# Performance work log

Measured on AMD Instinct MI355X. Metric: run time of the kernel, lower is better.

The kernel has to match this reference:

```python
import jax, jax.numpy as jnp
import numpy as np

DIM = 128
NUM_HEADS = 2
HEAD_DIM = DIM // NUM_HEADS
SCALE = HEAD_DIM ** -0.5
SR = 4
EPS_LN = 1e-5


def token2map(x, idx_token, H, W, H_init, W_init):
    """Scatter tokens x[B,N,Cc] into a [B,Cc,H,W] map via the init grid.
    Matches the sparse-COO branch of the torch token2map (N_init < N*H*W).
    """
    B, N, Cc = x.shape
    N_init = H_init * W_init
    # nearest-neighbor index of each init-grid cell in the HxW map
    rows = (jnp.arange(H_init) * H) // H_init          # floor(i * H / H_init)
    cols = (jnp.arange(W_init) * W) // W_init
    idx_hw = (rows[:, None] * W + cols[None, :]).reshape(-1)      # [N_init]
    flat = (idx_hw[None, :] + jnp.arange(B)[:, None] * (H * W)).reshape(-1)  # [B*N_init]
    # per-pixel count (A @ ones) + 1e-6, as in torch
    count = jax.ops.segment_sum(jnp.ones((B * N_init,), jnp.float32), flat,
                                num_segments=B * H * W) + 1e-6    # [B*H*W]
    gathered = jnp.take_along_axis(x, idx_token[..., None], axis=1)  # [B,N_init,Cc]
    out = jax.ops.segment_sum(gathered.reshape(B * N_init, Cc), flat,
                              num_segments=B * H * W)
    out = out / count[:, None]
    return out.reshape(B, H, W, Cc).transpose(0, 3, 1, 2)  # [B,Cc,H,W]


def setup_inputs() -> dict:
    key = jax.random.key(0)
    ks = jax.random.split(key, 12)
    B, Nq, Nkv, C = 8, 12544, 12544, DIM
    H, W, H_init, W_init = 112, 112, 224, 224
    inp = {
        'q_x': jax.random.normal(ks[0], (B, Nq, C), jnp.float32),
        'kv_x': jax.random.normal(ks[1], (B, Nkv, C), jnp.float32),
        'token_score': jax.random.normal(ks[2], (B, Nkv, 1), jnp.float32),
        'idx_token': jax.random.randint(ks[3], (B, H_init * W_init), 0, Nkv),
        'H': H, 'W': W, 'H_init': H_init, 'W_init': W_init,
        # learned params (qkv_bias=False)
        'q_w': jax.random.normal(ks[4], (C, C), jnp.float32) * 0.02,
        'kv_w': jax.random.normal(ks[5], (C, 2 * C), jnp.float32) * 0.02,
        'proj_w': jax.random.normal(ks[6], (C, C), jnp.float32) * 0.02,
        'proj_b': jnp.zeros((C,), jnp.float32),
        'sr_w': jax.random.normal(ks[7], (C, C, SR, SR), jnp.float32) * np.sqrt(2.0 / (SR * SR * C)),
        'sr_b': jnp.zeros((C,), jnp.float32),
        'norm_g': jnp.ones((C,), jnp.float32),
        'norm_b': jnp.zeros((C,), jnp.float32),
    }
    return inp


def reference(q_x, kv_x, token_score, q_w, kv_w, proj_w, proj_b, sr_w, sr_b,
              norm_g, norm_b, idx_token, H, W, H_init, W_init):
    B, Nq, C = q_x.shape
    # q projection -> [B, h, Nq, d]
    q = (q_x @ q_w).reshape(B, Nq, NUM_HEADS, HEAD_DIM).transpose(0, 2, 1, 3)

    # sr_ratio > 1 path: scatter kv tokens (with conf channel) to q's map
    tmp = jnp.concatenate([kv_x, token_score], axis=-1)          # [B,Nkv,C+1]
    tmp_map = token2map(tmp, idx_token, H, W, H_init, W_init)    # [B,C+1,H,W]
    kv_map = tmp_map[:, :C]                                      # [B,C,H,W]
    conf_map = tmp_map[:, C:]                                    # [B,1,H,W]

    # spatial reduction conv (kernel=stride=SR) + LayerNorm
    kv_r = jax.lax.conv_general_dilated(
        kv_map, sr_w, window_strides=(SR, SR), padding='VALID',
        dimension_numbers=('NCHW', 'OIHW', 'NCHW')) + sr_b[None, :, None, None]
    h, w = kv_r.shape[2], kv_r.shape[3]
    Ns = h * w
    kv_t = kv_r.reshape(B, C, Ns).transpose(0, 2, 1)             # [B,Ns,C]
    mu = jnp.mean(kv_t, axis=-1, keepdims=True)
    var = jnp.mean(jnp.square(kv_t - mu), axis=-1, keepdims=True)
    kv_t = (kv_t - mu) / jnp.sqrt(var + EPS_LN) * norm_g + norm_b

    # avg-pool conf to the reduced grid
    conf = conf_map.reshape(B, 1, h, SR, w, SR).mean(axis=(3, 5)).reshape(B, Ns)

    # kv projection -> k,v [B,h,Ns,d]
    kv_p = (kv_t @ kv_w).reshape(B, Ns, 2, NUM_HEADS, HEAD_DIM).transpose(2, 0, 3, 1, 4)
    k, v = kv_p[0], kv_p[1]

    attn = jnp.einsum('bhqd,bhkd->bhqk', q * SCALE, k) + conf[:, None, None, :]
    attn = jax.nn.softmax(attn, axis=-1)
    out = jnp.einsum('bhqk,bhkd->bhqd', attn, v).transpose(0, 2, 1, 3).reshape(B, Nq, C)
    return out @ proj_w + proj_b
```

## Files before the change

### kernel.cpp

```cpp
#include <hip/hip_runtime.h>
#include <hip/hip_bf16.h>


#define NBATCH 8
#define NQTOK  12544
#define NSP    832
#define LOG2E  1.4426950408889634f
#define QSCALE (0.125f * LOG2E)

typedef __attribute__((ext_vector_type(8))) short bf8;
typedef __attribute__((ext_vector_type(4))) float f4;
typedef __attribute__((ext_vector_type(4))) unsigned short u16x4;
typedef __attribute__((ext_vector_type(2))) unsigned int u32x2;

#define MFMA16(a, b, c) __builtin_amdgcn_mfma_f32_16x16x32_bf16((a), (b), (c), 0, 0, 0)

#if __has_builtin(__builtin_amdgcn_exp2f)
#define EXP2(x) __builtin_amdgcn_exp2f(x)
#else
#define EXP2(x) exp2f(x)
#endif

__device__ __forceinline__ unsigned short f2b(float x) {
  union { float f; unsigned u; } v; v.f = x;
  unsigned r = v.u + 0x7FFFu + ((v.u >> 16) & 1u);
  return (unsigned short)(r >> 16);
}

__device__ __forceinline__ unsigned pk2(float lo, float hi) {
  float2 t; t.x = lo; t.y = hi;
  __hip_bfloat162 bb = __float22bfloat162_rn(t);
  union { __hip_bfloat162 b; unsigned u; } v; v.b = bb;
  return v.u;
}

__device__ __forceinline__ bf8 ldfrag(const unsigned short* t, int stride, int rbase, int kbase) {
  int lane = threadIdx.x & 63;
  return *(const bf8*)(t + (rbase + (lane & 15)) * stride + kbase + ((lane >> 4) << 3));
}

__global__ void k_setup(const float* __restrict__ qw, const float* __restrict__ kvw,
                        const float* __restrict__ pw, const float* __restrict__ srw,
                        unsigned short* __restrict__ qwt, unsigned short* __restrict__ kvwt,
                        unsigned short* __restrict__ pwt, unsigned short* __restrict__ srwt,
                        unsigned* __restrict__ kb, unsigned* __restrict__ vb,
                        float* __restrict__ conf) {
  int tid = blockIdx.x * 256 + threadIdx.x;
  int nt = gridDim.x * 256;
  for (int i = tid; i < 128 * 128; i += nt) {
    int k = i >> 7, n = i & 127;
    qwt[n * 128 + k] = f2b(qw[k * 128 + n]);
    pwt[n * 128 + k] = f2b(pw[k * 128 + n]);
  }
  for (int i = tid; i < 128 * 256; i += nt) {
    int k = i >> 8, j = i & 255;
    kvwt[j * 128 + k] = f2b(kvw[k * 256 + j]);
  }
  for (int i = tid; i < 128 * 2048; i += nt) {
    int o = i >> 11, kk = i & 2047;
    int p = kk >> 7, c = kk & 127;
    srwt[o * 2048 + kk] = f2b(srw[o * 2048 + c * 16 + p]);
  }
  const int nu = NBATCH * 2 * NSP * 64 / 2;
  for (int i = tid; i < nu; i += nt) { kb[i] = 0u; vb[i] = 0u; }
  for (int i = tid; i < NBATCH * NSP; i += nt) conf[i] = -1e30f;
}

__global__ void k_token2map(const float* __restrict__ kv_x, const float* __restrict__ tsc,
                            const int* __restrict__ idxt,
                            unsigned short* __restrict__ kv_map, float* __restrict__ conf_map) {
  int half = threadIdx.x >> 7;
  int c = threadIdx.x & 127;
  int cell = blockIdx.x * 2 + half;
  int b = cell / 12544, hw = cell - b * 12544;
  int h = hw / 112, w = hw - h * 112;
  const int* it = idxt + b * 50176;
  int t0 = it[(2 * h) * 224 + 2 * w];
  int t1 = it[(2 * h) * 224 + 2 * w + 1];
  int t2 = it[(2 * h + 1) * 224 + 2 * w];
  int t3 = it[(2 * h + 1) * 224 + 2 * w + 1];
  const float* base = kv_x + (long)b * 12544 * 128;
  const float recip = 1.0f / (4.0f + 1e-6f);
  float s = base[t0 * 128 + c] + base[t1 * 128 + c] + base[t2 * 128 + c] + base[t3 * 128 + c];
  kv_map[(long)cell * 128 + c] = f2b(s * recip);
  if (c == 0) {
    const float* ts = tsc + b * 12544;
    conf_map[cell] = (ts[t0] + ts[t1] + ts[t2] + ts[t3]) * recip;
  }
}

__launch_bounds__(256)
__global__ void k_conv_ln(const unsigned short* __restrict__ kv_map,
                          const unsigned short* __restrict__ srwt,
                          const float* __restrict__ srb, const float* __restrict__ ng,
                          const float* __restrict__ nb, unsigned short* __restrict__ kv_t,
                          const float* __restrict__ conf_map, float* __restrict__ conf) {
  __shared__ unsigned short At[64 * 136];
  __shared__ unsigned short Bt[128 * 136];
  const int tid = threadIdx.x;
  const int lane = tid & 63, w = tid >> 6;
  const int l15 = lane & 15, g = lane >> 4;
  const int r0 = blockIdx.x * 64;
  if (tid < 64) {
    int pos = r0 + tid;
    int bq = pos / 784, p2 = pos - bq * 784;
    int oh = p2 / 28, ow = p2 - oh * 28;
    float s = 0.f;
#pragma unroll
    for (int kh = 0; kh < 4; kh++)
#pragma unroll
      for (int kw = 0; kw < 4; kw++)
        s += conf_map[bq * 12544 + (4 * oh + kh) * 112 + 4 * ow + kw];
    conf[bq * NSP + p2] = s * (LOG2E / 16.0f);
  }
  const f4 fz = {0.f, 0.f, 0.f, 0.f};
  f4 acc[8];
#pragma unroll
  for (int i = 0; i < 8; i++) acc[i] = fz;

  for (int p = 0; p < 16; p++) {
#pragma unroll
    for (int j = 0; j < 4; j++) {
      int id = tid + 256 * j;
      int row = id >> 4, c0 = (id & 15) << 3;
      int rr = r0 + row;
      int bb = rr / 784, pos = rr - bb * 784;
      int oh = pos / 28, ow = pos - oh * 28;
      long src = ((long)(bb * 12544 + (4 * oh + (p >> 2)) * 112 + 4 * ow + (p & 3))) * 128 + c0;
      *(uint4*)(At + row * 136 + c0) = *(const uint4*)(kv_map + src);
    }
#pragma unroll
    for (int j = 0; j < 8; j++) {
      int id = tid + 256 * j;
      int row = id >> 4, c0 = (id & 15) << 3;
      *(uint4*)(Bt + row * 136 + c0) = *(const uint4*)(srwt + row * 2048 + p * 128 + c0);
    }
    __syncthreads();
#pragma unroll
    for (int ks = 0; ks < 4; ks++) {
      bf8 a = ldfrag(At, 136, 16 * w, 32 * ks);
#pragma unroll
      for (int nf = 0; nf < 8; nf++) {
        bf8 bb = ldfrag(Bt, 136, 16 * nf, 32 * ks);
        acc[nf] = MFMA16(a, bb, acc[nf]);
      }
    }
    __syncthreads();
  }
  float sum_[4] = {0.f, 0.f, 0.f, 0.f}, sq_[4] = {0.f, 0.f, 0.f, 0.f};
#pragma unroll
  for (int nf = 0; nf < 8; nf++) {
    float bias = srb[16 * nf + l15];
#pragma unroll
    for (int reg = 0; reg < 4; reg++) {
      float v = acc[nf][reg] + bias;
      acc[nf][reg] = v;
      sum_[reg] += v;
      sq_[reg] += v * v;
    }
  }
#pragma unroll
  for (int msk = 1; msk < 16; msk <<= 1)
#pragma unroll
    for (int reg = 0; reg < 4; reg++) {
      sum_[reg] += __shfl_xor(sum_[reg], msk, 64);
      sq_[reg] += __shfl_xor(sq_[reg], msk, 64);
    }
  float mean[4], rstd[4];
#pragma unroll
  for (int reg = 0; reg < 4; reg++) {
    mean[reg] = sum_[reg] * (1.0f / 128.0f);
    float var = sq_[reg] * (1.0f / 128.0f) - mean[reg] * mean[reg];
    rstd[reg] = rsqrtf(var + 1e-5f);
  }
#pragma unroll
  for (int nf = 0; nf < 8; nf++) {
    float gc = ng[16 * nf + l15], bc = nb[16 * nf + l15];
#pragma unroll
    for (int reg = 0; reg < 4; reg++) {
      int row = r0 + 16 * w + 4 * g + reg;
      float v = (acc[nf][reg] - mean[reg]) * rstd[reg] * gc + bc;
      kv_t[row * 128 + 16 * nf + l15] = f2b(v);
    }
  }
}

__launch_bounds__(256)
__global__ void k_kv(const unsigned short* __restrict__ kv_t,
                     const unsigned short* __restrict__ kvwt,
                     unsigned short* __restrict__ kbuf, unsigned short* __restrict__ vbuf) {
  __shared__ unsigned short At[64 * 136];
  __shared__ unsigned short Bt[128 * 136];
  const int tid = threadIdx.x;
  const int lane = tid & 63, w = tid >> 6;
  const int l15 = lane & 15, g = lane >> 4;
  const int r0 = blockIdx.x * 64;
  const int sel = blockIdx.y;
#pragma unroll
  for (int j = 0; j < 4; j++) {
    int id = tid + 256 * j;
    int row = id >> 4, c0 = (id & 15) << 3;
    *(uint4*)(At + row * 136 + c0) = *(const uint4*)(kv_t + (long)(r0 + row) * 128 + c0);
  }
#pragma unroll
  for (int j = 0; j < 8; j++) {
    int id = tid + 256 * j;
    int row = id >> 4, c0 = (id & 15) << 3;
    *(uint4*)(Bt + row * 136 + c0) = *(const uint4*)(kvwt + (long)(sel * 128 + row) * 128 + c0);
  }
  __syncthreads();
  const f4 fz = {0.f, 0.f, 0.f, 0.f};
  f4 acc[8];
#pragma unroll
  for (int i = 0; i < 8; i++) acc[i] = fz;
#pragma unroll
  for (int ks = 0; ks < 4; ks++) {
    bf8 a = ldfrag(At, 136, 16 * w, 32 * ks);
#pragma unroll
    for (int nf = 0; nf < 8; nf++) {
      bf8 bb = ldfrag(Bt, 136, 16 * nf, 32 * ks);
      acc[nf] = MFMA16(a, bb, acc[nf]);
    }
  }
#pragma unroll
  for (int nf = 0; nf < 8; nf++)
#pragma unroll
    for (int reg = 0; reg < 4; reg++) {
      int r = r0 + 16 * w + 4 * g + reg;
      int b = r / 784, ns = r - b * 784;
      int j = 16 * nf + l15;
      int hh = j >> 6, d = j & 63;
      unsigned short val = f2b(acc[nf][reg]);
      if (sel == 0) kbuf[((long)(b * 2 + hh) * NSP + ns) * 64 + d] = val;
      else          vbuf[((long)(b * 2 + hh) * 64 + d) * NSP + ns] = val;
    }
}

__launch_bounds__(256)
__global__ void k_q(const float* __restrict__ q_x, const unsigned short* __restrict__ qwt,
                    unsigned short* __restrict__ qbuf) {
  __shared__ unsigned short At[64 * 136];
  __shared__ unsigned short Bt[128 * 136];
  const int tid = threadIdx.x;
  const int lane = tid & 63, w = tid >> 6;
  const int l15 = lane & 15, g = lane >> 4;
  const int r0 = blockIdx.x * 64;
#pragma unroll
  for (int j = 0; j < 8; j++) {
    int id = tid + 256 * j;
    int row = id >> 5, c0 = (id & 31) << 2;
    float4 v = *(const float4*)(q_x + (long)(r0 + row) * 128 + c0);
    u16x4 o;
    o[0] = f2b(v.x); o[1] = f2b(v.y); o[2] = f2b(v.z); o[3] = f2b(v.w);
    *(u16x4*)(At + row * 136 + c0) = o;
  }
#pragma unroll
  for (int j = 0; j < 8; j++) {
    int id = tid + 256 * j;
    int row = id >> 4, c0 = (id & 15) << 3;
    *(uint4*)(Bt + row * 136 + c0) = *(const uint4*)(qwt + (long)row * 128 + c0);
  }
  __syncthreads();
  const f4 fz = {0.f, 0.f, 0.f, 0.f};
  f4 acc[8];
#pragma unroll
  for (int i = 0; i < 8; i++) acc[i] = fz;
#pragma unroll
  for (int ks = 0; ks < 4; ks++) {
    bf8 a = ldfrag(At, 136, 16 * w, 32 * ks);
#pragma unroll
    for (int nf = 0; nf < 8; nf++) {
      bf8 bb = ldfrag(Bt, 136, 16 * nf, 32 * ks);
      acc[nf] = MFMA16(a, bb, acc[nf]);
    }
  }
#pragma unroll
  for (int nf = 0; nf < 8; nf++)
#pragma unroll
    for (int reg = 0; reg < 4; reg++) {
      int r = r0 + 16 * w + 4 * g + reg;
      int b = r / NQTOK, n = r - b * NQTOK;
      int j = 16 * nf + l15;
      int hh = j >> 6, d = j & 63;
      qbuf[((long)(b * 2 + hh) * NQTOK + n) * 64 + d] = f2b(acc[nf][reg] * QSCALE);
    }
}

__launch_bounds__(256, 3)
__global__ void k_attn(const unsigned short* __restrict__ qbuf,
                       const unsigned short* __restrict__ kbuf,
                       const unsigned short* __restrict__ vbuf,
                       const float* __restrict__ conf,
                       unsigned short* __restrict__ attbuf) {
  __shared__ unsigned short Kt[2][64 * 72];
  __shared__ unsigned short Vt[2][64 * 72];
  const int tid = threadIdx.x;
  const int lane = tid & 63, w = tid >> 6;
  const int l15 = lane & 15, g = lane >> 4;
  const int h = blockIdx.y, b = blockIdx.z;
  const int bh = b * 2 + h;
  const int q0 = blockIdx.x * 128 + 32 * w;

  const unsigned short* qsrc = qbuf + ((long)bh * NQTOK + q0) * 64;
  bf8 qf[2][2];
#pragma unroll
  for (int mr = 0; mr < 2; mr++)
#pragma unroll
    for (int ks = 0; ks < 2; ks++)
      qf[mr][ks] = *(const bf8*)(qsrc + (16 * mr + l15) * 64 + 32 * ks + (g << 3));

  const int srow = tid >> 2;
  const int scol = (tid & 3) << 4;
  const unsigned short* kg = kbuf + (long)bh * NSP * 64 + srow * 64 + scol;
  const unsigned short* vg = vbuf + (long)bh * 64 * NSP + (long)srow * NSP + scol;
  unsigned short* klds = &Kt[0][0] + srow * 72 + scol;
  unsigned short* vlds = &Vt[0][0] + srow * 72 + scol;

  uint4 kr0, kr1, vr0, vr1;
#define ISSUE(T)                                                   \
  do {                                                             \
    const unsigned short* kp_ = kg + (long)(T) * 4096;             \
    const unsigned short* vp_ = vg + (T) * 64;                     \
    kr0 = *(const uint4*)(kp_);                                    \
    kr1 = *(const uint4*)(kp_ + 8);                                \
    vr0 = *(const uint4*)(vp_);                                    \
    vr1 = *(const uint4*)(vp_ + 8);                                \
  } while (0)
#define STWRITE(BUF)                                               \
  do {                                                             \
    unsigned short* kd_ = klds + (BUF) * 4608;                     \
    unsigned short* vd_ = vlds + (BUF) * 4608;                     \
    *(uint4*)kd_ = kr0;  *(uint4*)(kd_ + 8) = kr1;                 \
    *(uint4*)vd_ = vr0;  *(uint4*)(vd_ + 8) = vr1;                 \
  } while (0)

  ISSUE(0);
  STWRITE(0);
  ISSUE(1);
  __syncthreads();

  const f4 fz = {0.f, 0.f, 0.f, 0.f};
  f4 ao[2][4], aol[2];
#pragma unroll
  for (int mr = 0; mr < 2; mr++) {
    aol[mr] = fz;
#pragma unroll
    for (int i = 0; i < 4; i++) ao[mr][i] = fz;
  }
  const short on = (short)0x3F80;
  const bf8 onesf = {on, on, on, on, on, on, on, on};
  const float* confb = conf + b * NSP;

#pragma unroll 2
  for (int t = 0; t < 13; t++) {
    const int cur = t & 1;
    const unsigned short* KtB = &Kt[cur][0];
    const unsigned short* VtB = &Vt[cur][0];
    bf8 kf[4][2];
#pragma unroll
    for (int mf = 0; mf < 4; mf++)
#pragma unroll
      for (int ks = 0; ks < 2; ks++)
        kf[mf][ks] = ldfrag(KtB, 72, 16 * mf, 32 * ks);
    bf8 vf[4][2];
#pragma unroll
    for (int nfd = 0; nfd < 4; nfd++)
#pragma unroll
      for (int ks = 0; ks < 2; ks++)
        vf[nfd][ks] = ldfrag(VtB, 72, 16 * nfd, 32 * ks);
    float4 cv[4];
#pragma unroll
    for (int mf = 0; mf < 4; mf++)
      cv[mf] = *(const float4*)(confb + t * 64 + 16 * mf + 4 * g);
#pragma unroll
    for (int mr = 0; mr < 2; mr++) {
      f4 s_[4];
#pragma unroll
      for (int mf = 0; mf < 4; mf++) s_[mf] = fz;
#pragma unroll
      for (int ks = 0; ks < 2; ks++)
#pragma unroll
        for (int mf = 0; mf < 4; mf++)
          s_[mf] = MFMA16(kf[mf][ks], qf[mr][ks], s_[mf]);
      unsigned W[4][2];
#pragma unroll
      for (int mf = 0; mf < 4; mf++) {
        float p0 = EXP2(s_[mf][0] + cv[mf].x);
        float p1 = EXP2(s_[mf][1] + cv[mf].y);
        float p2 = EXP2(s_[mf][2] + cv[mf].z);
        float p3 = EXP2(s_[mf][3] + cv[mf].w);
        W[mf][0] = pk2(p0, p1);
        W[mf][1] = pk2(p2, p3);
      }
#pragma unroll
      for (int ks = 0; ks < 2; ks++) {
        u32x2 r0 = __builtin_amdgcn_permlane32_swap(W[2 * ks][0], W[2 * ks + 1][0], false, false);
        u32x2 t02 = __builtin_amdgcn_permlane16_swap(r0.x, r0.y, false, false);
        u32x2 r1 = __builtin_amdgcn_permlane32_swap(W[2 * ks][1], W[2 * ks + 1][1], false, false);
        u32x2 t13 = __builtin_amdgcn_permlane16_swap(r1.x, r1.y, false, false);
        union { unsigned u[4]; bf8 v; } pa;
        pa.u[0] = t02.x; pa.u[1] = t13.x; pa.u[2] = t02.y; pa.u[3] = t13.y;
        aol[mr] = MFMA16(pa.v, onesf, aol[mr]);
#pragma unroll
        for (int nfd = 0; nfd < 4; nfd++)
          ao[mr][nfd] = MFMA16(pa.v, vf[nfd][ks], ao[mr][nfd]);
      }
    }
    if (t < 12) STWRITE(cur ^ 1);
    if (t < 11) ISSUE(t + 2);
    __syncthreads();
  }
#undef ISSUE
#undef STWRITE
#pragma unroll
  for (int mr = 0; mr < 2; mr++) {
    float inv[4];
#pragma unroll
    for (int reg = 0; reg < 4; reg++) inv[reg] = 1.0f / aol[mr][reg];
#pragma unroll
    for (int nfd = 0; nfd < 4; nfd++)
#pragma unroll
      for (int reg = 0; reg < 4; reg++) {
        int n = q0 + 16 * mr + 4 * g + reg;
        int col = h * 64 + 16 * nfd + l15;
        attbuf[((long)b * NQTOK + n) * 128 + col] = f2b(ao[mr][nfd][reg] * inv[reg]);
      }
  }
}

__launch_bounds__(256)
__global__ void k_proj(const unsigned short* __restrict__ attbuf,
                       const unsigned short* __restrict__ pwt,
                       const float* __restrict__ pb, float* __restrict__ out) {
  __shared__ unsigned short At[64 * 136];
  __shared__ unsigned short Bt[128 * 136];
  const int tid = threadIdx.x;
  const int lane = tid & 63, w = tid >> 6;
  const int l15 = lane & 15, g = lane >> 4;
  const int r0 = blockIdx.x * 64;
#pragma unroll
  for (int j = 0; j < 4; j++) {
    int id = tid + 256 * j;
    int row = id >> 4, c0 = (id & 15) << 3;
    *(uint4*)(At + row * 136 + c0) = *(const uint4*)(attbuf + (long)(r0 + row) * 128 + c0);
  }
#pragma unroll
  for (int j = 0; j < 8; j++) {
    int id = tid + 256 * j;
    int row = id >> 4, c0 = (id & 15) << 3;
    *(uint4*)(Bt + row * 136 + c0) = *(const uint4*)(pwt + (long)row * 128 + c0);
  }
  __syncthreads();
  const f4 fz = {0.f, 0.f, 0.f, 0.f};
  f4 acc[8];
#pragma unroll
  for (int i = 0; i < 8; i++) acc[i] = fz;
#pragma unroll
  for (int ks = 0; ks < 4; ks++) {
    bf8 a = ldfrag(At, 136, 16 * w, 32 * ks);
#pragma unroll
    for (int nf = 0; nf < 8; nf++) {
      bf8 bb = ldfrag(Bt, 136, 16 * nf, 32 * ks);
      acc[nf] = MFMA16(a, bb, acc[nf]);
    }
  }
#pragma unroll
  for (int nf = 0; nf < 8; nf++) {
    float bias = pb[16 * nf + l15];
#pragma unroll
    for (int reg = 0; reg < 4; reg++) {
      int r = r0 + 16 * w + 4 * g + reg;
      out[(long)r * 128 + 16 * nf + l15] = acc[nf][reg] + bias;
    }
  }
}

extern "C" void kernel_launch(void* const* d_in, const int* in_sizes, int n_in,
                              void* d_out, int out_size, void* d_ws, size_t ws_size,
                              hipStream_t stream) {
  const float* q_x  = (const float*)d_in[0];
  const float* kv_x = (const float*)d_in[1];
  const float* tsc  = (const float*)d_in[2];
  const int*   idxt = (const int*)d_in[3];
  const float* q_w  = (const float*)d_in[8];
  const float* kv_w = (const float*)d_in[9];
  const float* pw   = (const float*)d_in[10];
  const float* pb   = (const float*)d_in[11];
  const float* srw  = (const float*)d_in[12];
  const float* srb  = (const float*)d_in[13];
  const float* ng   = (const float*)d_in[14];
  const float* nb   = (const float*)d_in[15];
  float* outp = (float*)d_out;

  char* ws = (char*)d_ws;
  size_t off = 0;
  auto take = [&](size_t bytes) {
    char* p = ws + off;
    off += (bytes + 255) & ~(size_t)255;
    return p;
  };
  unsigned short* qwt   = (unsigned short*)take(128 * 128 * 2);
  unsigned short* pwt   = (unsigned short*)take(128 * 128 * 2);
  unsigned short* kvwt  = (unsigned short*)take(256 * 128 * 2);
  unsigned short* srwt  = (unsigned short*)take(128 * 2048 * 2);
  unsigned short* kvmap = (unsigned short*)take((size_t)NBATCH * 12544 * 128 * 2);
  float* conf_map       = (float*)take((size_t)NBATCH * 12544 * 4);
  unsigned short* kvt   = (unsigned short*)take((size_t)NBATCH * 784 * 128 * 2);
  unsigned short* kbuf  = (unsigned short*)take((size_t)NBATCH * 2 * NSP * 64 * 2);
  unsigned short* vbuf  = (unsigned short*)take((size_t)NBATCH * 2 * NSP * 64 * 2);
  float* conf           = (float*)take((size_t)NBATCH * NSP * 4);
  unsigned short* qbuf  = (unsigned short*)take((size_t)NBATCH * 2 * NQTOK * 64 * 2);
  unsigned short* attbuf = kvmap;

  k_setup<<<512, 256, 0, stream>>>(q_w, kv_w, pw, srw, qwt, kvwt, pwt, srwt,
                                   (unsigned*)kbuf, (unsigned*)vbuf, conf);
  k_token2map<<<50176, 256, 0, stream>>>(kv_x, tsc, idxt, kvmap, conf_map);
  k_conv_ln<<<98, 256, 0, stream>>>(kvmap, srwt, srb, ng, nb, kvt, conf_map, conf);
  k_kv<<<dim3(98, 2), 256, 0, stream>>>(kvt, kvwt, kbuf, vbuf);
  k_q<<<1568, 256, 0, stream>>>(q_x, qwt, qbuf);
  k_attn<<<dim3(98, 2, 8), 256, 0, stream>>>(qbuf, kbuf, vbuf, conf, attbuf);
  k_proj<<<1568, 256, 0, stream>>>(attbuf, pwt, pb, outp);
}
```

Before: 178.4 us.

## Fuse conv+LN with KV projection, vectorize token2map, remap attention blocks to XCDs

Merges the conv+LayerNorm kernel with the KV projection, so normalized rows stay in shared memory and B fragments come straight from global memory, dropping one launch and the kv_t round trip. token2map now uses float4 loads with 32 threads per cell and batch-interleaved block ids, and the Q scale is folded into the transposed weight. Attention blocks use a 1-D grid mapped so that each XCD handles one batch's two heads, aiming to improve L2 locality of K/V. The fused kernel keeps more accumulators (16 f4), which raises register pressure.

```diff
diff --git a/kernel.cpp b/kernel.cpp
--- a/kernel.cpp
+++ b/kernel.cpp
@@ -32,6 +32,16 @@
   __hip_bfloat162 bb = __float22bfloat162_rn(t);
   union { __hip_bfloat162 b; unsigned u; } v; v.b = bb;
   return v.u;
+}
+
+__device__ __forceinline__ bf8 rows2frag(const unsigned W0[2], const unsigned W1[2]) {
+  u32x2 r0 = __builtin_amdgcn_permlane32_swap(W0[0], W1[0], false, false);
+  u32x2 t02 = __builtin_amdgcn_permlane16_swap(r0.x, r0.y, false, false);
+  u32x2 r1 = __builtin_amdgcn_permlane32_swap(W0[1], W1[1], false, false);
+  u32x2 t13 = __builtin_amdgcn_permlane16_swap(r1.x, r1.y, false, false);
+  union { unsigned u[4]; bf8 v; } pa;
+  pa.u[0] = t02.x; pa.u[1] = t13.x; pa.u[2] = t02.y; pa.u[3] = t13.y;
+  return pa.v;
 }
 
 __device__ __forceinline__ bf8 ldfrag(const unsigned short* t, int stride, int rbase, int kbase) {
@@ -49,7 +59,7 @@
   int nt = gridDim.x * 256;
   for (int i = tid; i < 128 * 128; i += nt) {
     int k = i >> 7, n = i & 127;
-    qwt[n * 128 + k] = f2b(qw[k * 128 + n]);
+    qwt[n * 128 + k] = f2b(qw[k * 128 + n] * QSCALE);
     pwt[n * 128 + k] = f2b(pw[k * 128 + n]);
   }
   for (int i = tid; i < 128 * 256; i += nt) {
@@ -69,32 +79,45 @@
 __global__ void k_token2map(const float* __restrict__ kv_x, const float* __restrict__ tsc,
                             const int* __restrict__ idxt,
                             unsigned short* __restrict__ kv_map, float* __restrict__ conf_map) {
-  int half = threadIdx.x >> 7;
-  int c = threadIdx.x & 127;
-  int cell = blockIdx.x * 2 + half;
-  int b = cell / 12544, hw = cell - b * 12544;
+  int tid = threadIdx.x;
+  int bid = blockIdx.x;
+  int b = bid & 7, pos = bid >> 3;
+  int hw = pos * 8 + (tid >> 5);
+  int cell = b * 12544 + hw;
+  int c0 = (tid & 31) << 2;
   int h = hw / 112, w = hw - h * 112;
   const int* it = idxt + b * 50176;
   int t0 = it[(2 * h) * 224 + 2 * w];
   int t1 = it[(2 * h) * 224 + 2 * w + 1];
   int t2 = it[(2 * h + 1) * 224 + 2 * w];
   int t3 = it[(2 * h + 1) * 224 + 2 * w + 1];
-  const float* base = kv_x + (long)b * 12544 * 128;
+  const float* base = kv_x + (long)b * 12544 * 128 + c0;
   const float recip = 1.0f / (4.0f + 1e-6f);
-  float s = base[t0 * 128 + c] + base[t1 * 128 + c] + base[t2 * 128 + c] + base[t3 * 128 + c];
-  kv_map[(long)cell * 128 + c] = f2b(s * recip);
-  if (c == 0) {
+  float4 a0 = *(const float4*)(base + (long)t0 * 128);
+  float4 a1 = *(const float4*)(base + (long)t1 * 128);
+  float4 a2 = *(const float4*)(base + (long)t2 * 128);
+  float4 a3 = *(const float4*)(base + (long)t3 * 128);
+  u16x4 o;
+  o[0] = f2b((a0.x + a1.x + a2.x + a3.x) * recip);
+  o[1] = f2b((a0.y + a1.y + a2.y + a3.y) * recip);
+  o[2] = f2b((a0.z + a1.z + a2.z + a3.z) * recip);
+  o[3] = f2b((a0.w + a1.w + a2.w + a3.w) * recip);
+  *(u16x4*)(kv_map + (long)cell * 128 + c0) = o;
+  if ((tid & 31) == 0) {
     const float* ts = tsc + b * 12544;
     conf_map[cell] = (ts[t0] + ts[t1] + ts[t2] + ts[t3]) * recip;
   }
 }
 
 __launch_bounds__(256)
-__global__ void k_conv_ln(const unsigned short* __restrict__ kv_map,
-                          const unsigned short* __restrict__ srwt,
-                          const float* __restrict__ srb, const float* __restrict__ ng,
-                          const float* __restrict__ nb, unsigned short* __restrict__ kv_t,
-                          const float* __restrict__ conf_map, float* __restrict__ conf) {
+__global__ void k_conv_ln_kv(const unsigned short* __restrict__ kv_map,
+                             const unsigned short* __restrict__ srwt,
+                             const float* __restrict__ srb, const float* __restrict__ ng,
+                             const float* __restrict__ nb,
+                             const unsigned short* __restrict__ kvwt,
+                             unsigned short* __restrict__ kbuf,
+                             unsigned short* __restrict__ vbuf,
+                             const float* __restrict__ conf_map, float* __restrict__ conf) {
   __shared__ unsigned short At[64 * 136];
   __shared__ unsigned short Bt[128 * 136];
   const int tid = threadIdx.x;
@@ -166,71 +189,39 @@
       sum_[reg] += __shfl_xor(sum_[reg], msk, 64);
       sq_[reg] += __shfl_xor(sq_[reg], msk, 64);
     }
-  float mean[4], rstd[4];
-#pragma unroll
-  for (int reg = 0; reg < 4; reg++) {
-    mean[reg] = sum_[reg] * (1.0f / 128.0f);
-    float var = sq_[reg] * (1.0f / 128.0f) - mean[reg] * mean[reg];
-    rstd[reg] = rsqrtf(var + 1e-5f);
-  }
 #pragma unroll
   for (int nf = 0; nf < 8; nf++) {
     float gc = ng[16 * nf + l15], bc = nb[16 * nf + l15];
 #pragma unroll
     for (int reg = 0; reg < 4; reg++) {
-      int row = r0 + 16 * w + 4 * g + reg;
-      float v = (acc[nf][reg] - mean[reg]) * rstd[reg] * gc + bc;
-      kv_t[row * 128 + 16 * nf + l15] = f2b(v);
-    }
-  }
-}
-
-__launch_bounds__(256)
-__global__ void k_kv(const unsigned short* __restrict__ kv_t,
-                     const unsigned short* __restrict__ kvwt,
-                     unsigned short* __restrict__ kbuf, unsigned short* __restrict__ vbuf) {
-  __shared__ unsigned short At[64 * 136];
-  __shared__ unsigned short Bt[128 * 136];
-  const int tid = threadIdx.x;
-  const int lane = tid & 63, w = tid >> 6;
-  const int l15 = lane & 15, g = lane >> 4;
-  const int r0 = blockIdx.x * 64;
-  const int sel = blockIdx.y;
-#pragma unroll
-  for (int j = 0; j < 4; j++) {
-    int id = tid + 256 * j;
-    int row = id >> 4, c0 = (id & 15) << 3;
-    *(uint4*)(At + row * 136 + c0) = *(const uint4*)(kv_t + (long)(r0 + row) * 128 + c0);
-  }
-#pragma unroll
-  for (int j = 0; j < 8; j++) {
-    int id = tid + 256 * j;
-    int row = id >> 4, c0 = (id & 15) << 3;
-    *(uint4*)(Bt + row * 136 + c0) = *(const uint4*)(kvwt + (long)(sel * 128 + row) * 128 + c0);
+      float mean = sum_[reg] * (1.0f / 128.0f);
+      float var = sq_[reg] * (1.0f / 128.0f) - mean * mean;
+      float v = (acc[nf][reg] - mean) * rsqrtf(var + 1e-5f) * gc + bc;
+      At[(16 * w + 4 * g + reg) * 136 + 16 * nf + l15] = f2b(v);
+    }
   }
   __syncthreads();
-  const f4 fz = {0.f, 0.f, 0.f, 0.f};
-  f4 acc[8];
-#pragma unroll
-  for (int i = 0; i < 8; i++) acc[i] = fz;
+  f4 acc2[16];
+#pragma unroll
+  for (int i = 0; i < 16; i++) acc2[i] = fz;
 #pragma unroll
   for (int ks = 0; ks < 4; ks++) {
     bf8 a = ldfrag(At, 136, 16 * w, 32 * ks);
 #pragma unroll
-    for (int nf = 0; nf < 8; nf++) {
-      bf8 bb = ldfrag(Bt, 136, 16 * nf, 32 * ks);
-      acc[nf] = MFMA16(a, bb, acc[nf]);
-    }
-  }
-#pragma unroll
-  for (int nf = 0; nf < 8; nf++)
+    for (int nf = 0; nf < 16; nf++) {
+      bf8 bb = *(const bf8*)(kvwt + (16 * nf + l15) * 128 + 32 * ks + (g << 3));
+      acc2[nf] = MFMA16(a, bb, acc2[nf]);
+    }
+  }
+#pragma unroll
+  for (int nf = 0; nf < 16; nf++)
 #pragma unroll
     for (int reg = 0; reg < 4; reg++) {
       int r = r0 + 16 * w + 4 * g + reg;
       int b = r / 784, ns = r - b * 784;
       int j = 16 * nf + l15;
-      int hh = j >> 6, d = j & 63;
-      unsigned short val = f2b(acc[nf][reg]);
+      int sel = j >> 7, hh = (j >> 6) & 1, d = j & 63;
+      unsigned short val = f2b(acc2[nf][reg]);
       if (sel == 0) kbuf[((long)(b * 2 + hh) * NSP + ns) * 64 + d] = val;
       else          vbuf[((long)(b * 2 + hh) * 64 + d) * NSP + ns] = val;
     }
@@ -282,7 +273,7 @@
       int b = r / NQTOK, n = r - b * NQTOK;
       int j = 16 * nf + l15;
       int hh = j >> 6, d = j & 63;
-      qbuf[((long)(b * 2 + hh) * NQTOK + n) * 64 + d] = f2b(acc[nf][reg] * QSCALE);
+      qbuf[((long)(b * 2 + hh) * NQTOK + n) * 64 + d] = f2b(acc[nf][reg]);
     }
 }
 
@@ -297,9 +288,14 @@
   const int tid = threadIdx.x;
   const int lane = tid & 63, w = tid >> 6;
   const int l15 = lane & 15, g = lane >> 4;
-  const int h = blockIdx.y, b = blockIdx.z;
+  const int bid = blockIdx.x;
+  const int xcd = bid & 7, idx = bid >> 3;
+  const int sub = idx / 98;
+  const int xb = idx - sub * 98;
+  const int bhid = xcd * 2 + sub;
+  const int b = bhid >> 1, h = bhid & 1;
   const int bh = b * 2 + h;
-  const int q0 = blockIdx.x * 128 + 32 * w;
+  const int q0 = xb * 128 + 32 * w;
 
   const unsigned short* qsrc = qbuf + ((long)bh * NQTOK + q0) * 64;
   bf8 qf[2][2];
@@ -394,16 +390,11 @@
       }
 #pragma unroll
       for (int ks = 0; ks < 2; ks++) {
-        u32x2 r0 = __builtin_amdgcn_permlane32_swap(W[2 * ks][0], W[2 * ks + 1][0], false, false);
-        u32x2 t02 = __builtin_amdgcn_permlane16_swap(r0.x, r0.y, false, false);
-        u32x2 r1 = __builtin_amdgcn_permlane32_swap(W[2 * ks][1], W[2 * ks + 1][1], false, false);
-        u32x2 t13 = __builtin_amdgcn_permlane16_swap(r1.x, r1.y, false, false);
-        union { unsigned u[4]; bf8 v; } pa;
-        pa.u[0] = t02.x; pa.u[1] = t13.x; pa.u[2] = t02.y; pa.u[3] = t13.y;
-        aol[mr] = MFMA16(pa.v, onesf, aol[mr]);
+        bf8 pa = rows2frag(W[2 * ks], W[2 * ks + 1]);
+        aol[mr] = MFMA16(pa, onesf, aol[mr]);
 #pragma unroll
         for (int nfd = 0; nfd < 4; nfd++)
-          ao[mr][nfd] = MFMA16(pa.v, vf[nfd][ks], ao[mr][nfd]);
+          ao[mr][nfd] = MFMA16(pa, vf[nfd][ks], ao[mr][nfd]);
       }
     }
     if (t < 12) STWRITE(cur ^ 1);
@@ -505,7 +496,6 @@
   unsigned short* srwt  = (unsigned short*)take(128 * 2048 * 2);
   unsigned short* kvmap = (unsigned short*)take((size_t)NBATCH * 12544 * 128 * 2);
   float* conf_map       = (float*)take((size_t)NBATCH * 12544 * 4);
-  unsigned short* kvt   = (unsigned short*)take((size_t)NBATCH * 784 * 128 * 2);
   unsigned short* kbuf  = (unsigned short*)take((size_t)NBATCH * 2 * NSP * 64 * 2);
   unsigned short* vbuf  = (unsigned short*)take((size_t)NBATCH * 2 * NSP * 64 * 2);
   float* conf           = (float*)take((size_t)NBATCH * NSP * 4);
@@ -514,10 +504,10 @@
 
   k_setup<<<512, 256, 0, stream>>>(q_w, kv_w, pw, srw, qwt, kvwt, pwt, srwt,
                                    (unsigned*)kbuf, (unsigned*)vbuf, conf);
-  k_token2map<<<50176, 256, 0, stream>>>(kv_x, tsc, idxt, kvmap, conf_map);
-  k_conv_ln<<<98, 256, 0, stream>>>(kvmap, srwt, srb, ng, nb, kvt, conf_map, conf);
-  k_kv<<<dim3(98, 2), 256, 0, stream>>>(kvt, kvwt, kbuf, vbuf);
+  k_token2map<<<12544, 256, 0, stream>>>(kv_x, tsc, idxt, kvmap, conf_map);
+  k_conv_ln_kv<<<98, 256, 0, stream>>>(kvmap, srwt, srb, ng, nb, kvwt, kbuf, vbuf,
+                                       conf_map, conf);
   k_q<<<1568, 256, 0, stream>>>(q_x, qwt, qbuf);
-  k_attn<<<dim3(98, 2, 8), 256, 0, stream>>>(qbuf, kbuf, vbuf, conf, attbuf);
+  k_attn<<<1568, 256, 0, stream>>>(qbuf, kbuf, vbuf, conf, attbuf);
   k_proj<<<1568, 256, 0, stream>>>(attbuf, pwt, pb, outp);
 }
```

Result: faster. 161.0 us (-9.8%).
